# Performance work log

Hardware: AMD Instinct MI355X
Metric: run time of the kernel (lower is better)

The kernel has to match this reference:

```python
import jax, jax.numpy as jnp
import numpy as np

D_MODEL = 2048
HEADS = 16
HEAD_DIM = D_MODEL // HEADS  # 128


def setup_inputs() -> dict:
    key = jax.random.key(0)
    k1, k2, k3 = jax.random.split(key, 3)
    B, S = 1, 2048
    x = jax.random.normal(k1, (B, S, D_MODEL), dtype=jnp.float32)
    Wqkv_w = jax.random.normal(k2, (D_MODEL + 2 * HEAD_DIM, D_MODEL), dtype=jnp.float32) * (D_MODEL ** -0.5)
    Wqkv_b = jnp.zeros((D_MODEL + 2 * HEAD_DIM,), dtype=jnp.float32)
    out_w = jax.random.normal(k3, (D_MODEL, D_MODEL), dtype=jnp.float32) * (D_MODEL ** -0.5)
    out_b = jnp.zeros((D_MODEL,), dtype=jnp.float32)
    return {"x": x, "Wqkv_w": Wqkv_w, "Wqkv_b": Wqkv_b, "out_w": out_w, "out_b": out_b}


def reference(x, Wqkv_w, Wqkv_b, out_w, out_b):
    B, S, _ = x.shape
    # fused QKV projection
    qkv = jnp.einsum('bsd,ed->bse', x, Wqkv_w) + Wqkv_b  # [B,S,D+2*hd]
    q = qkv[..., :D_MODEL]                               # [B,S,D]
    k = qkv[..., D_MODEL:D_MODEL + HEAD_DIM]             # [B,S,hd] single KV head
    v = qkv[..., D_MODEL + HEAD_DIM:]                    # [B,S,hd]
    q = q.reshape(B, S, HEADS, HEAD_DIM)                 # [B,S,H,hd]
    scale = 1.0 / np.sqrt(HEAD_DIM)
    # QK^T with shared K head, scaled
    scores = jnp.einsum('bqhd,bkd->bhqk', q, k) * scale  # [B,H,S,S]
    # causal mask (additive fill with dtype min, matching masked_fill)
    min_val = jnp.finfo(scores.dtype).min
    causal = jnp.tril(jnp.ones((S, S), dtype=bool))
    scores = jnp.where(causal[None, None], scores, min_val)
    attn = jax.nn.softmax(scores, axis=-1)               # [B,H,S,S]
    ctx = jnp.einsum('bhqk,bkd->bqhd', attn, v)          # [B,S,H,hd]
    ctx = ctx.reshape(B, S, D_MODEL)
    out = jnp.einsum('bsd,ed->bse', ctx, out_w) + out_b  # [B,S,D]
    return out
```

## Files before the change

### kernel.cpp

```cpp
#include <hip/hip_runtime.h>
#include <hip/hip_bf16.h>
#include <math.h>


#define S_LEN 2048
#define DMODEL 2048
#define EQKV 2304
#define HDIM 128
#define NHEADS 16
#define VTS 2080

typedef _Float16 f16;
typedef __attribute__((ext_vector_type(8))) _Float16 f16x8;
typedef __attribute__((ext_vector_type(4))) _Float16 f16x4;
typedef __attribute__((ext_vector_type(4))) float f32x4;

#define MFMA16(a, b, c) __builtin_amdgcn_mfma_f32_16x16x32_f16((a), (b), (c), 0, 0, 0)

#define ALPHA 0.12751879526655967f
#define CFIX 10.0f

__device__ __forceinline__ void load_lds16(const void* g, void* l) {
  __builtin_amdgcn_global_load_lds((const __attribute__((address_space(1))) void*)g,
                                   (__attribute__((address_space(3))) void*)l, 16, 0, 0);
}

__global__ void f32_to_f16_kernel(const float* __restrict__ in, f16* __restrict__ out, int n4) {
  int i = blockIdx.x * blockDim.x + threadIdx.x;
  if (i < n4) {
    float4 v = reinterpret_cast<const float4*>(in)[i];
    f16x4 o = {(f16)v.x, (f16)v.y, (f16)v.z, (f16)v.w};
    reinterpret_cast<f16x4*>(out)[i] = o;
  }
}

template <typename OutT, bool QKV>
__global__ __launch_bounds__(256) void gemm_bt(
    const f16* __restrict__ A, const f16* __restrict__ Bm,
    const float* __restrict__ bias, OutT* __restrict__ C,
    f16* __restrict__ VT, int M, int N, int K) {
  __shared__ __align__(16) char smem[24576];
  const int tid = threadIdx.x;
  const int w = tid >> 6;
  const int l = tid & 63;
  const int bm = blockIdx.x, bn = blockIdx.y;
  const int wm = w >> 1, wn = w & 1;
  const int lg = l >> 4;
  const int lm = l & 15;
  const int l7 = l & 7;

  f32x4 acc[2][4] = {};

  int aoff[2][2], boff[4][2];
#pragma unroll
  for (int mf = 0; mf < 2; ++mf) {
    int row = wm * 32 + mf * 16 + lm;
#pragma unroll
    for (int kk = 0; kk < 2; ++kk)
      aoff[mf][kk] = row * 128 + ((kk * 4 + lg) ^ l7) * 16;
  }
#pragma unroll
  for (int nf = 0; nf < 4; ++nf) {
    int row = wn * 64 + nf * 16 + lm;
#pragma unroll
    for (int kk = 0; kk < 2; ++kk)
      boff[nf][kk] = 8192 + row * 128 + ((kk * 4 + lg) ^ l7) * 16;
  }

  const int nkt = K >> 6;
  for (int kt = 0; kt < nkt; ++kt) {
    const int k0 = kt << 6;
#pragma unroll
    for (int i = 0; i < 2; ++i) {
      int slot = i * 256 + w * 64 + l;
      int row = slot >> 3;
      int cg = (slot & 7) ^ (row & 7);
      const f16* g = A + (size_t)(bm * 64 + row) * K + k0 + cg * 8;
      load_lds16(g, smem + (i * 256 + w * 64) * 16);
    }
#pragma unroll
    for (int i = 0; i < 4; ++i) {
      int slot = i * 256 + w * 64 + l;
      int row = slot >> 3;
      int cg = (slot & 7) ^ (row & 7);
      const f16* g = Bm + (size_t)(bn * 128 + row) * K + k0 + cg * 8;
      load_lds16(g, smem + 8192 + (i * 256 + w * 64) * 16);
    }
    __syncthreads();
#pragma unroll
    for (int kk = 0; kk < 2; ++kk) {
      f16x8 af[2], bf[4];
#pragma unroll
      for (int mf = 0; mf < 2; ++mf)
        af[mf] = *reinterpret_cast<const f16x8*>(smem + aoff[mf][kk]);
#pragma unroll
      for (int nf = 0; nf < 4; ++nf)
        bf[nf] = *reinterpret_cast<const f16x8*>(smem + boff[nf][kk]);
#pragma unroll
      for (int mf = 0; mf < 2; ++mf)
#pragma unroll
        for (int nf = 0; nf < 4; ++nf)
          acc[mf][nf] = MFMA16(af[mf], bf[nf], acc[mf][nf]);
    }
    __syncthreads();
  }

#pragma unroll
  for (int mf = 0; mf < 2; ++mf) {
#pragma unroll
    for (int nf = 0; nf < 4; ++nf) {
      int col = bn * 128 + wn * 64 + nf * 16 + lm;
      float bv = bias[col];
#pragma unroll
      for (int j = 0; j < 4; ++j) {
        int row = bm * 64 + wm * 32 + mf * 16 + lg * 4 + j;
        float v = acc[mf][nf][j] + bv;
        if (QKV && col >= DMODEL + HDIM) {
          VT[(size_t)(col - DMODEL - HDIM) * VTS + row] = (f16)v;
        } else {
          C[(size_t)row * N + col] = (OutT)v;
        }
      }
    }
  }
}

__device__ __forceinline__ void stage_kv(const f16* __restrict__ qkv,
                                         const f16* __restrict__ vt, int k0,
                                         char* kb, char* vb, int tid, int wv) {
#pragma unroll
  for (int i = 0; i < 4; ++i) {
    int slot = i * 256 + tid;
    int r = slot >> 4;
    int cs = (slot & 15) ^ (r & 7);
    load_lds16(qkv + (size_t)(k0 + r) * EQKV + DMODEL + cs * 8,
               kb + (i * 256 + wv * 64) * 16);
  }
#pragma unroll
  for (int i = 0; i < 4; ++i) {
    int slot = i * 256 + tid;
    int d = slot >> 3;
    int cs = (slot & 7) ^ (d & 7);
    load_lds16(vt + (size_t)d * VTS + k0 + cs * 8,
               vb + (i * 256 + wv * 64) * 16);
  }
}

__global__ __launch_bounds__(256, 2) void flash_mha4(
    const f16* __restrict__ qkv, const f16* __restrict__ vt, f16* __restrict__ ctx,
    f16* __restrict__ Opart, float* __restrict__ lbuf) {
  const int qt32 = blockIdx.x;
  const int ch = blockIdx.y;
  const int hg = blockIdx.z;
  const int ktiles = (qt32 >> 1) + 1;
  if (ch * 8 >= ktiles) return;

  extern __shared__ char smem[];
  const int tid = threadIdx.x;
  const int wv = tid >> 6;
  const int l = tid & 63;
  const int lg = l >> 4, lm = l & 15;
  char* Pb = smem + 65536 + wv * 4096;
  const int head = hg * 4 + wv;
  const int wq0 = qt32 * 32;

  f16x8 qf[2][4];
#pragma unroll
  for (int mf = 0; mf < 2; ++mf)
#pragma unroll
    for (int ks = 0; ks < 4; ++ks)
      qf[mf][ks] = *reinterpret_cast<const f16x8*>(
          qkv + (size_t)(wq0 + mf * 16 + lm) * EQKV + head * HDIM + ks * 32 + lg * 8);

  f32x4 o[2][8] = {};
  float lsum[2][4] = {};

  const int kt0 = ch * 8;
  const int kt1 = min(ktiles, kt0 + 8);

  stage_kv(qkv, vt, kt0 * 64, smem, smem + 32768, tid, wv);
  int buf = 0;

  for (int t = kt0; t < kt1; ++t) {
    __syncthreads();
    char* kb = smem + buf * 16384;
    char* vb = smem + 32768 + buf * 16384;
    if (t + 1 < kt1)
      stage_kv(qkv, vt, (t + 1) * 64, smem + (buf ^ 1) * 16384,
               smem + 32768 + (buf ^ 1) * 16384, tid, wv);
    const int k0 = t * 64;

    f32x4 sc[2][4] = {};
#pragma unroll
    for (int ks = 0; ks < 4; ++ks) {
#pragma unroll
      for (int nf = 0; nf < 4; ++nf) {
        int row = nf * 16 + lm;
        int pos = (ks * 4 + lg) ^ (row & 7);
        f16x8 kf = *reinterpret_cast<const f16x8*>(kb + row * 256 + pos * 16);
        sc[0][nf] = MFMA16(qf[0][ks], kf, sc[0][nf]);
        sc[1][nf] = MFMA16(qf[1][ks], kf, sc[1][nf]);
      }
    }
    if (t == ktiles - 1) {
#pragma unroll
      for (int mf = 0; mf < 2; ++mf)
#pragma unroll
        for (int nf = 0; nf < 4; ++nf)
#pragma unroll
          for (int j = 0; j < 4; ++j) {
            int row = wq0 + mf * 16 + lg * 4 + j;
            int col = k0 + nf * 16 + lm;
            if (col > row) sc[mf][nf][j] = -__builtin_inff();
          }
    }
#pragma unroll
    for (int mf = 0; mf < 2; ++mf)
#pragma unroll
      for (int nf = 0; nf < 4; ++nf)
#pragma unroll
        for (int j = 0; j < 4; ++j) {
          float p = exp2f(sc[mf][nf][j] * ALPHA - CFIX);
          lsum[mf][j] += p;
          int prow = mf * 16 + lg * 4 + j;
          int c = nf * 2 + (lm >> 3);
          *reinterpret_cast<f16*>(Pb + prow * 128 + ((c ^ (prow & 7)) * 16 + (lm & 7) * 2)) = (f16)p;
        }
    asm volatile("s_waitcnt lgkmcnt(0)" ::: "memory");
    __builtin_amdgcn_sched_barrier(0);
#pragma unroll
    for (int kk = 0; kk < 2; ++kk) {
      f16x8 pa[2];
#pragma unroll
      for (int mf = 0; mf < 2; ++mf) {
        int prow = mf * 16 + lm;
        int pos = (kk * 4 + lg) ^ (prow & 7);
        pa[mf] = *reinterpret_cast<const f16x8*>(Pb + prow * 128 + pos * 16);
      }
#pragma unroll
      for (int df = 0; df < 8; ++df) {
        int d = df * 16 + lm;
        int pos = (kk * 4 + lg) ^ (d & 7);
        f16x8 vf = *reinterpret_cast<const f16x8*>(vb + d * 128 + pos * 16);
        o[0][df] = MFMA16(pa[0], vf, o[0][df]);
        o[1][df] = MFMA16(pa[1], vf, o[1][df]);
      }
    }
    buf ^= 1;
  }

#pragma unroll
  for (int mf = 0; mf < 2; ++mf)
#pragma unroll
    for (int j = 0; j < 4; ++j) {
#pragma unroll
      for (int d = 1; d < 16; d <<= 1) lsum[mf][j] += __shfl_xor(lsum[mf][j], d);
    }

  if (qt32 < 16) {
#pragma unroll
    for (int mf = 0; mf < 2; ++mf)
#pragma unroll
      for (int j = 0; j < 4; ++j) {
        float inv = 1.0f / lsum[mf][j];
        int row = wq0 + mf * 16 + lg * 4 + j;
#pragma unroll
        for (int df = 0; df < 8; ++df)
          ctx[(size_t)row * DMODEL + head * HDIM + df * 16 + lm] =
              (f16)(o[mf][df][j] * inv);
      }
  } else {
    const int slot = head * 192 + (qt32 - 16) * 4 + ch;
    f16* Op = Opart + (size_t)slot * 4096;
    float* lp = lbuf + (size_t)slot * 32;
#pragma unroll
    for (int mf = 0; mf < 2; ++mf)
#pragma unroll
      for (int j = 0; j < 4; ++j) {
        int rl = mf * 16 + lg * 4 + j;
#pragma unroll
        for (int df = 0; df < 8; ++df)
          Op[rl * 128 + df * 16 + lm] = (f16)o[mf][df][j];
        if (lm == 0) lp[rl] = lsum[mf][j];
      }
  }
}

__global__ __launch_bounds__(128) void flash_combine(
    const f16* __restrict__ Opart, const float* __restrict__ lbuf,
    f16* __restrict__ ctx) {
  const int qt32 = blockIdx.x, head = blockIdx.y;
  if (qt32 < 16) return;
  const int ktiles = (qt32 >> 1) + 1;
  const int nch = (ktiles + 7) >> 3;
  const int tid = threadIdx.x;
  const int row = tid >> 2, cg = tid & 3;
  const int slot0 = head * 192 + (qt32 - 16) * 4;

  float L = 0.f;
  for (int i = 0; i < nch; ++i) L += lbuf[(size_t)(slot0 + i) * 32 + row];
  const float invL = 1.0f / L;
  const int rowg = qt32 * 32 + row;

#pragma unroll
  for (int g = 0; g < 4; ++g) {
    float acc[8] = {0.f, 0.f, 0.f, 0.f, 0.f, 0.f, 0.f, 0.f};
    for (int i = 0; i < nch; ++i) {
      f16x8 v = *reinterpret_cast<const f16x8*>(
          Opart + (size_t)(slot0 + i) * 4096 + row * 128 + cg * 32 + g * 8);
#pragma unroll
      for (int j = 0; j < 8; ++j) acc[j] += (float)v[j];
    }
    f16x8 ov;
#pragma unroll
    for (int j = 0; j < 8; ++j) ov[j] = (f16)(acc[j] * invL);
    *reinterpret_cast<f16x8*>(ctx + (size_t)rowg * DMODEL + head * HDIM + cg * 32 + g * 8) = ov;
  }
}

extern "C" void kernel_launch(void* const* d_in, const int* in_sizes, int n_in,
                              void* d_out, int out_size, void* d_ws, size_t ws_size,
                              hipStream_t stream) {
  const float* x = (const float*)d_in[0];
  const float* Wqkv_w = (const float*)d_in[1];
  const float* Wqkv_b = (const float*)d_in[2];
  const float* out_w = (const float*)d_in[3];
  const float* out_b = (const float*)d_in[4];

  char* p = (char*)d_ws;
  f16* xh = (f16*)p;    p += (size_t)S_LEN * DMODEL * 2;
  f16* wqh = (f16*)p;   p += (size_t)EQKV * DMODEL * 2;
  f16* owh = (f16*)p;   p += (size_t)DMODEL * DMODEL * 2;
  f16* qkvh = (f16*)p;  p += (size_t)S_LEN * EQKV * 2;
  f16* vth = (f16*)p;   p += (size_t)HDIM * VTS * 2;
  f16* ctxh = (f16*)p;  p += (size_t)S_LEN * DMODEL * 2;
  f16* Opart = (f16*)p;   p += (size_t)3072 * 4096 * 2;
  float* lbuf = (float*)p; p += (size_t)3072 * 32 * 4;

  f32_to_f16_kernel<<<(S_LEN * DMODEL / 4) / 256, 256, 0, stream>>>(x, xh, S_LEN * DMODEL / 4);
  f32_to_f16_kernel<<<(EQKV * DMODEL / 4) / 256, 256, 0, stream>>>(Wqkv_w, wqh, EQKV * DMODEL / 4);
  f32_to_f16_kernel<<<(DMODEL * DMODEL / 4) / 256, 256, 0, stream>>>(out_w, owh, DMODEL * DMODEL / 4);

  gemm_bt<f16, true><<<dim3(S_LEN / 64, EQKV / 128), 256, 0, stream>>>(
      xh, wqh, Wqkv_b, qkvh, vth, S_LEN, EQKV, DMODEL);

  flash_mha4<<<dim3(64, 4, 4), 256, 81920, stream>>>(qkvh, vth, ctxh, Opart, lbuf);
  flash_combine<<<dim3(64, 16), 128, 0, stream>>>(Opart, lbuf, ctxh);

  gemm_bt<float, false><<<dim3(S_LEN / 64, DMODEL / 128), 256, 0, stream>>>(
      ctxh, owh, out_b, (float*)d_out, nullptr, S_LEN, DMODEL, DMODEL);
}
```

Measured before the change: 221.9 us.

## Double-buffer GEMM LDS tiles and merge the three f32-to-f16 cast launches

The GEMM main loop now prefetches the next K tile into a second LDS buffer while MFMAs run on the current one, so each iteration needs one barrier instead of two. This is meant to hide global-to-LDS load latency. LDS per block doubles to 48 KB, which may lower occupancy. Separately, the three cast kernels become a single launch that picks its source by flat index and writes into the contiguous f16 workspace, removing two launch overheads.

```diff
diff --git a/kernel.cpp b/kernel.cpp
--- a/kernel.cpp
+++ b/kernel.cpp
@@ -25,12 +25,38 @@
                                    (__attribute__((address_space(3))) void*)l, 16, 0, 0);
 }
 
-__global__ void f32_to_f16_kernel(const float* __restrict__ in, f16* __restrict__ out, int n4) {
+__global__ void cast3_kernel(const float* __restrict__ a, const float* __restrict__ b,
+                             const float* __restrict__ c, f16* __restrict__ dst) {
   int i = blockIdx.x * blockDim.x + threadIdx.x;
-  if (i < n4) {
-    float4 v = reinterpret_cast<const float4*>(in)[i];
-    f16x4 o = {(f16)v.x, (f16)v.y, (f16)v.z, (f16)v.w};
-    reinterpret_cast<f16x4*>(out)[i] = o;
+  const float* src;
+  int off;
+  if (i < 1048576) { src = a; off = 0; }
+  else if (i < 1048576 + 1179648) { src = b; off = 1048576; }
+  else { src = c; off = 1048576 + 1179648; }
+  float4 v = reinterpret_cast<const float4*>(src)[i - off];
+  f16x4 o = {(f16)v.x, (f16)v.y, (f16)v.z, (f16)v.w};
+  reinterpret_cast<f16x4*>(dst)[i] = o;
+}
+
+__device__ __forceinline__ void gemm_stage(const f16* __restrict__ A,
+                                           const f16* __restrict__ Bm,
+                                           int bm, int bn, int K, int k0,
+                                           char* base, int w, int l) {
+#pragma unroll
+  for (int i = 0; i < 2; ++i) {
+    int slot = i * 256 + w * 64 + l;
+    int row = slot >> 3;
+    int cg = (slot & 7) ^ (row & 7);
+    load_lds16(A + (size_t)(bm * 64 + row) * K + k0 + cg * 8,
+               base + (i * 256 + w * 64) * 16);
+  }
+#pragma unroll
+  for (int i = 0; i < 4; ++i) {
+    int slot = i * 256 + w * 64 + l;
+    int row = slot >> 3;
+    int cg = (slot & 7) ^ (row & 7);
+    load_lds16(Bm + (size_t)(bn * 128 + row) * K + k0 + cg * 8,
+               base + 8192 + (i * 256 + w * 64) * 16);
   }
 }
 
@@ -39,7 +65,7 @@
     const f16* __restrict__ A, const f16* __restrict__ Bm,
     const float* __restrict__ bias, OutT* __restrict__ C,
     f16* __restrict__ VT, int M, int N, int K) {
-  __shared__ __align__(16) char smem[24576];
+  __shared__ __align__(16) char smem[49152];
   const int tid = threadIdx.x;
   const int w = tid >> 6;
   const int l = tid & 63;
@@ -68,34 +94,22 @@
   }
 
   const int nkt = K >> 6;
+  gemm_stage(A, Bm, bm, bn, K, 0, smem, w, l);
+  __syncthreads();
+  int buf = 0;
   for (int kt = 0; kt < nkt; ++kt) {
-    const int k0 = kt << 6;
-#pragma unroll
-    for (int i = 0; i < 2; ++i) {
-      int slot = i * 256 + w * 64 + l;
-      int row = slot >> 3;
-      int cg = (slot & 7) ^ (row & 7);
-      const f16* g = A + (size_t)(bm * 64 + row) * K + k0 + cg * 8;
-      load_lds16(g, smem + (i * 256 + w * 64) * 16);
-    }
-#pragma unroll
-    for (int i = 0; i < 4; ++i) {
-      int slot = i * 256 + w * 64 + l;
-      int row = slot >> 3;
-      int cg = (slot & 7) ^ (row & 7);
-      const f16* g = Bm + (size_t)(bn * 128 + row) * K + k0 + cg * 8;
-      load_lds16(g, smem + 8192 + (i * 256 + w * 64) * 16);
-    }
-    __syncthreads();
+    char* cur = smem + buf * 24576;
+    if (kt + 1 < nkt)
+      gemm_stage(A, Bm, bm, bn, K, (kt + 1) << 6, smem + (buf ^ 1) * 24576, w, l);
 #pragma unroll
     for (int kk = 0; kk < 2; ++kk) {
       f16x8 af[2], bf[4];
 #pragma unroll
       for (int mf = 0; mf < 2; ++mf)
-        af[mf] = *reinterpret_cast<const f16x8*>(smem + aoff[mf][kk]);
+        af[mf] = *reinterpret_cast<const f16x8*>(cur + aoff[mf][kk]);
 #pragma unroll
       for (int nf = 0; nf < 4; ++nf)
-        bf[nf] = *reinterpret_cast<const f16x8*>(smem + boff[nf][kk]);
+        bf[nf] = *reinterpret_cast<const f16x8*>(cur + boff[nf][kk]);
 #pragma unroll
       for (int mf = 0; mf < 2; ++mf)
 #pragma unroll
@@ -103,6 +117,7 @@
           acc[mf][nf] = MFMA16(af[mf], bf[nf], acc[mf][nf]);
     }
     __syncthreads();
+    buf ^= 1;
   }
 
 #pragma unroll
@@ -337,9 +352,7 @@
   f16* Opart = (f16*)p;   p += (size_t)3072 * 4096 * 2;
   float* lbuf = (float*)p; p += (size_t)3072 * 32 * 4;
 
-  f32_to_f16_kernel<<<(S_LEN * DMODEL / 4) / 256, 256, 0, stream>>>(x, xh, S_LEN * DMODEL / 4);
-  f32_to_f16_kernel<<<(EQKV * DMODEL / 4) / 256, 256, 0, stream>>>(Wqkv_w, wqh, EQKV * DMODEL / 4);
-  f32_to_f16_kernel<<<(DMODEL * DMODEL / 4) / 256, 256, 0, stream>>>(out_w, owh, DMODEL * DMODEL / 4);
+  cast3_kernel<<<12800, 256, 0, stream>>>(x, Wqkv_w, out_w, xh);
 
   gemm_bt<f16, true><<<dim3(S_LEN / 64, EQKV / 128), 256, 0, stream>>>(
       xh, wqh, Wqkv_b, qkvh, vth, S_LEN, EQKV, DMODEL);
```

New measurement: 211.5 us. 4.7% less time.
